# Kernel optimization log

Measured on AMD Instinct MI355X. Metric: run time of the kernel, lower is better.

The kernel has to match this reference:

```python
import jax, jax.numpy as jnp
import numpy as np

B, T, E, H = 32, 256, 1024, 1024


def setup_inputs() -> dict:
    key = jax.random.key(0)
    ks = jax.random.split(key, 8)
    stdv = 1.0 / np.sqrt(H)
    u = lambda k, shape: jax.random.uniform(k, shape, jnp.float32, -stdv, stdv)
    return {
        "x": jax.random.normal(ks[0], (B, T, E), jnp.float32),
        "mask": jnp.ones((B, T), jnp.float32),
        "W_ih0": u(ks[1], (E, 4 * H)),
        "W_hh0": u(ks[2], (H, 4 * H)),
        "b0": jnp.zeros((4 * H,), jnp.float32),
        "W_ih1": u(ks[3], (H, 4 * H)),
        "W_hh1": u(ks[4], (H, 4 * H)),
        "b1": jnp.zeros((4 * H,), jnp.float32),
    }


def _cell(inp, m_t, h0, c0, Wih, Whh, b):
    # pre-activations: [B, 4H]; gate order f, i, o, g (as in torch.split)
    pre = inp @ Wih + h0 @ Whh + b
    f, i, o, g = jnp.split(pre, 4, axis=1)
    m = m_t[:, None]
    c1 = jax.nn.sigmoid(f) * c0 + jax.nn.sigmoid(i) * jnp.tanh(g)
    c1 = c1 * m + c0 * (1.0 - m)
    h1 = jax.nn.sigmoid(o) * jnp.tanh(c1)
    h1 = h1 * m + h0 * (1.0 - m)
    return h1, c1


def reference(x, mask, W_ih0, W_hh0, b0, W_ih1, W_hh1, b1):
    Bz = x.shape[0]
    Hd = W_hh0.shape[0]

    def step(carry, xm):
        h0, c0, h1, c1 = carry
        xt, mt = xm
        # NOTE: layer 1 consumes PREVIOUS timestep's layer-0 hidden (source quirk)
        nh1, nc1 = _cell(h0, mt, h1, c1, W_ih1, W_hh1, b1)
        nh0, nc0 = _cell(xt, mt, h0, c0, W_ih0, W_hh0, b0)
        return (nh0, nc0, nh1, nc1), nh1

    z = jnp.zeros((Bz, Hd), x.dtype)
    init = (z, z, z, z)
    xs = (jnp.swapaxes(x, 0, 1), jnp.swapaxes(mask, 0, 1))  # [T,B,E], [T,B]
    _, hs = jax.lax.scan(step, init, xs)  # hs: [T, B, H]
    states = jnp.swapaxes(hs, 0, 1)  # [B, T, H]
    return states, mask
```

## Files before the change

kernel.cpp:

```cpp
#include <hip/hip_runtime.h>
#include <hip/hip_bf16.h>
#include <stdint.h>
#include <stddef.h>

#define TT    256
#define NBLK  128

typedef __attribute__((ext_vector_type(8))) short short8;
typedef __attribute__((ext_vector_type(4))) float f32x4;

__device__ __forceinline__ short f2bf(float v) {
  uint32_t u = __builtin_bit_cast(uint32_t, v);
  uint32_t r = (u + 0x7fffu + ((u >> 16) & 1u)) >> 16;
  return (short)r;
}

__device__ __forceinline__ void stage_coh(const short8* g, short8* l) {
  __builtin_amdgcn_global_load_lds(
      (const __attribute__((address_space(1))) void*)g,
      (__attribute__((address_space(3))) void*)l, 16, 0, 17);
}
__device__ __forceinline__ void stage_pln(const short8* g, short8* l) {
  __builtin_amdgcn_global_load_lds(
      (const __attribute__((address_space(1))) void*)g,
      (__attribute__((address_space(3))) void*)l, 16, 0, 0);
}

__device__ __forceinline__ void spin_lines(const uint32_t* baseA, uint32_t tgtA,
                                           const uint32_t* baseB, uint32_t tgtB,
                                           int lane) {
  const uint32_t* p = (lane < 32 ? baseA : baseB) + (lane & 15) * 32;
  const uint32_t tgt = (lane < 32) ? tgtA : tgtB;
  for (;;) {
    uint32_t v = __hip_atomic_load(p, __ATOMIC_RELAXED, __HIP_MEMORY_SCOPE_AGENT);
    if (__all(v >= tgt)) break;
    __builtin_amdgcn_s_sleep(1);
  }
}

__global__ void k_init(const float* __restrict__ mask, float* __restrict__ out,
                       uint32_t* __restrict__ z) {
  int tid = blockIdx.x * blockDim.x + threadIdx.x;
  if (tid < 8192) out[8388608 + tid] = mask[tid];
  for (int j = tid; j < 51200; j += 16384) z[j] = 0;
}

__global__ void k_packw(const float* __restrict__ Wih0, const float* __restrict__ Whh0,
                        const float* __restrict__ Wih1, const float* __restrict__ Whh1,
                        short* __restrict__ Bp) {
  int cid = blockIdx.x * blockDim.x + threadIdx.x;
  int l    = cid & 63;
  int f    = (cid >> 6) & 63;
  int wgid = cid >> 12;
  int q  = l >> 4, cc = l & 15;
  int cg = f >> 4, s = f & 15;
  int w    = wgid & 3;
  int blk  = (wgid >> 2) & 63;
  bool p1  = (wgid >= 256);
  int precol = (cc >> 2) * 1024 + blk * 16 + cg * 4 + (cc & 3);
  const float* MA = p1 ? Wih1 : Wih0;
  const float* MB = p1 ? Whh1 : Whh0;
  short8 o;
#pragma unroll
  for (int j = 0; j < 8; ++j) {
    int k = w * 512 + s * 32 + q * 8 + j;
    const float* M = (k < 1024) ? MA : MB;
    o[j] = f2bf(M[(size_t)(k & 1023) * 4096 + precol]);
  }
  ((short8*)Bp)[cid] = o;
}

__global__ void k_packx(const float* __restrict__ x, short* __restrict__ Xb) {
  int tid = blockIdx.x * blockDim.x + threadIdx.x;
  int eg = tid & 127;
  int t  = (tid >> 7) & 255;
  int b  = tid >> 15;
  const float* src = x + ((size_t)(b * 256 + t) * 1024 + eg * 8);
  short8 o;
#pragma unroll
  for (int j = 0; j < 8; ++j) o[j] = f2bf(src[j]);
  ((short8*)Xb)[(t * 128 + eg) * 32 + b] = o;
}

__global__ __launch_bounds__(256, 1) void k_lstm(
    const float* __restrict__ mask, const float* __restrict__ b0,
    const float* __restrict__ b1,   const short* __restrict__ Bp,
    const short* __restrict__ Xb,   short* __restrict__ h0r,
    short* __restrict__ h1b,        float* __restrict__ out,
    uint32_t* bar) {
  __shared__ short8 stg[8192];
  __shared__ f32x4 xch[4][3][2][64];
  __shared__ short hstage[512];

  const int tid  = threadIdx.x;
  const int wv   = tid >> 6;
  const int lane = tid & 63;
  const int quad = lane >> 4;
  const int cc   = lane & 15;
  const int bid  = blockIdx.x;
  const bool is1 = (bid >= 64);
  const int blk  = bid & 63;
  const int wgid = (is1 ? 256 : 0) + blk * 4 + wv;
  const int n0w  = blk * 16 + wv * 4;
  const int hcol = n0w + (cc & 3);
  const int kb0  = (wv & 1) * 64;
  const bool coh = !(!is1 && wv < 2);

  uint32_t* const lines0 = bar;
  uint32_t* const lines1 = bar + 1024;
  uint32_t* const arrC   = (is1 ? lines1 : lines0) + (blk & 15) * 32;

  short8 bfr[64];
  {
    const short8* pB = ((const short8*)Bp) + (size_t)wgid * 4096 + lane;
#pragma unroll
    for (int f = 0; f < 64; ++f) bfr[f] = pB[f * 64];
  }
  const float* bias = is1 ? b1 : b0;
  const float bv = bias[(cc >> 2) * 1024 + n0w + (cc & 3)];

  float cst[8], hst[8];
#pragma unroll
  for (int i = 0; i < 8; ++i) { cst[i] = 0.f; hst[i] = 0.f; }

  const int shuf_base = (lane & 48) | (lane & 3);
  const short8* Xq = (const short8*)Xb;
  const short8* H0 = (const short8*)h0r;
  const short8* H1 = (const short8*)h1b;

  short8* const ldsW = stg + wv * 2048;

  const int tmax = is1 ? TT : (TT - 1);

  for (int t = 0; t < tmax; ++t) {
    const int p  = t & 1;
    const int rs = (t + 127) & 127;

    const short8* pan;
    if (!is1) pan = (wv < 2) ? (Xq + (size_t)t * 4096) : (H0 + (size_t)rs * 4096);
    else      pan = (wv < 2) ? (H0 + (size_t)rs * 4096) : (H1 + p * 4096);

    float mrow[8];
#pragma unroll
    for (int i = 0; i < 8; ++i) {
      int r = ((i >> 2) << 4) + quad * 4 + (i & 3);
      mrow[i] = mask[r * 256 + t];
    }

    if (t > 0) {
      const uint32_t tgt = (uint32_t)(4 * t);
      if (!is1) {
        if (wv >= 2) {
          uint32_t tgtB = (t >= 127) ? (uint32_t)(4 * (t - 126)) : 0u;
          spin_lines(lines0, tgt, lines1, tgtB, lane);
        }
      } else {
        if (wv < 2) spin_lines(lines0, tgt, lines0, tgt, lane);
        else        spin_lines(lines1, tgt, lines1, tgt, lane);
      }
    }

    {
      const short8* gsrc = pan + kb0 * 32 + lane;
      if (coh) {
#pragma unroll
        for (int i = 0; i < 32; ++i) stage_coh(gsrc + i * 64, ldsW + i * 64);
      } else {
#pragma unroll
        for (int i = 0; i < 32; ++i) stage_pln(gsrc + i * 64, ldsW + i * 64);
      }
      asm volatile("s_waitcnt vmcnt(0)" ::: "memory");
      __builtin_amdgcn_sched_barrier(0);
    }

    f32x4 acc[4][2];
#pragma unroll
    for (int cg = 0; cg < 4; ++cg) { acc[cg][0] = (f32x4)0.f; acc[cg][1] = (f32x4)0.f; }

#pragma unroll
    for (int s = 0; s < 16; ++s) {
      short8 a0 = ldsW[(s * 4 + quad) * 32 + cc];
      short8 a1 = ldsW[(s * 4 + quad) * 32 + cc + 16];
#pragma unroll
      for (int cg = 0; cg < 4; ++cg) {
        acc[cg][0] = __builtin_amdgcn_mfma_f32_16x16x32_bf16(a0, bfr[cg * 16 + s], acc[cg][0], 0, 0, 0);
        acc[cg][1] = __builtin_amdgcn_mfma_f32_16x16x32_bf16(a1, bfr[cg * 16 + s], acc[cg][1], 0, 0, 0);
      }
    }

#pragma unroll
    for (int cg = 0; cg < 4; ++cg) {
      if (cg != wv) {
        int slot = cg < wv ? cg : cg - 1;
        xch[wv][slot][0][lane] = acc[cg][0];
        xch[wv][slot][1][lane] = acc[cg][1];
      }
    }
    __syncthreads();
    f32x4 s0 = acc[wv][0], s1 = acc[wv][1];
#pragma unroll
    for (int w2 = 0; w2 < 4; ++w2) {
      if (w2 != wv) {
        int slot = wv < w2 ? wv : wv - 1;
        s0 += xch[w2][slot][0][lane];
        s1 += xch[w2][slot][1][lane];
      }
    }

    float pv[8];
    pv[0] = s0.x + bv; pv[1] = s0.y + bv; pv[2] = s0.z + bv; pv[3] = s0.w + bv;
    pv[4] = s1.x + bv; pv[5] = s1.y + bv; pv[6] = s1.z + bv; pv[7] = s1.w + bv;

#pragma unroll
    for (int i = 0; i < 8; ++i) {
      float v = pv[i];
      float fg = __shfl(v, shuf_base + 0, 64);
      float ig = __shfl(v, shuf_base + 4, 64);
      float og = __shfl(v, shuf_base + 8, 64);
      float gg = __shfl(v, shuf_base + 12, 64);
      int r = ((i >> 2) << 4) + quad * 4 + (i & 3);
      float m  = mrow[i];
      float om = 1.f - m;
      float sf = 1.f / (1.f + __expf(-fg));
      float si = 1.f / (1.f + __expf(-ig));
      float so = 1.f / (1.f + __expf(-og));
      float e2 = __expf(-2.f * fabsf(gg));
      float tg = (1.f - e2) / (1.f + e2);
      tg = (gg < 0.f) ? -tg : tg;
      float c1 = sf * cst[i] + si * tg;
      c1 = c1 * m + cst[i] * om;
      float ec = __expf(-2.f * fabsf(c1));
      float tc = (1.f - ec) / (1.f + ec);
      tc = (c1 < 0.f) ? -tc : tc;
      float h1 = so * tc;
      h1 = h1 * m + hst[i] * om;
      cst[i] = c1; hst[i] = h1;
      if ((lane & 12) == 0) {
        int hl = wv * 4 + (cc & 3);
        hstage[(hl >> 3) * 256 + r * 8 + (hl & 7)] = f2bf(h1);
        if (is1) out[((size_t)r * 256 + t) * 1024 + hcol] = h1;
      }
    }

    if (is1 && t == TT - 1) break;

    __syncthreads();
    if (wv == 0) {
      short* dst = (is1 ? (h1b + (1 - p) * 32768)
                        : (h0r + (t & 127) * 32768)) + blk * 512 + lane * 8;
      short8 hv = ((const short8*)hstage)[lane];
      asm volatile("global_store_dwordx4 %0, %1, off sc0 sc1"
                   :: "v"(dst), "v"(hv) : "memory");
      if (lane == 0) {
        asm volatile("s_waitcnt vmcnt(0)" ::: "memory");
        __hip_atomic_fetch_add(arrC, 1u, __ATOMIC_RELAXED, __HIP_MEMORY_SCOPE_AGENT);
      }
    }
  }
}

extern "C" void kernel_launch(void* const* d_in, const int* in_sizes, int n_in,
                              void* d_out, int out_size, void* d_ws, size_t ws_size,
                              hipStream_t stream) {
  const float* x    = (const float*)d_in[0];
  const float* mask = (const float*)d_in[1];
  const float* Wih0 = (const float*)d_in[2];
  const float* Whh0 = (const float*)d_in[3];
  const float* b0   = (const float*)d_in[4];
  const float* Wih1 = (const float*)d_in[5];
  const float* Whh1 = (const float*)d_in[6];
  const float* b1   = (const float*)d_in[7];
  float* out = (float*)d_out;

  char* ws = (char*)d_ws;
  short*    Bp  = (short*)ws;
  short*    Xb  = (short*)(ws + 33554432);
  short*    h0r = (short*)(ws + 50331648);
  short*    h1b = (short*)(ws + 58720256);
  uint32_t* bar = (uint32_t*)(ws + 58851328);
  uint32_t* z   = (uint32_t*)(ws + 58654720);

  hipLaunchKernelGGL(k_init,  dim3(64),   dim3(256), 0, stream, mask, out, z);
  hipLaunchKernelGGL(k_packw, dim3(8192), dim3(256), 0, stream, Wih0, Whh0, Wih1, Whh1, Bp);
  hipLaunchKernelGGL(k_packx, dim3(4096), dim3(256), 0, stream, x, Xb);
  hipLaunchKernelGGL(k_lstm,  dim3(NBLK), dim3(256), 0, stream,
                     mask, b0, b1, Bp, Xb, h0r, h1b, out, bar);
}
```

Before: 2.555 ms.

## Replace coherent staging loads with ring buffers plus periodic acquire fence

The h1 buffer grows from a 2-entry double buffer into a 32-slot ring. All LDS staging loads now use plain cached global_load_lds instead of the coherent (sc-bit) variant. An agent-scope acquire fence every 32 steps invalidates stale cache lines, since each ring slot is only reused after 32 steps. This trades per-load cache bypass for an occasional fence and more workspace. It relies on the h0 ring (128 slots) and h1 ring (32 slots) never being served stale from cache between fences, which is a fragile memory-model assumption.

Result: faster. 2.475 ms (-3.1%).

```diff
diff --git a/kernel.cpp b/kernel.cpp
--- a/kernel.cpp
+++ b/kernel.cpp
@@ -15,12 +15,7 @@
   return (short)r;
 }
 
-__device__ __forceinline__ void stage_coh(const short8* g, short8* l) {
-  __builtin_amdgcn_global_load_lds(
-      (const __attribute__((address_space(1))) void*)g,
-      (__attribute__((address_space(3))) void*)l, 16, 0, 17);
-}
-__device__ __forceinline__ void stage_pln(const short8* g, short8* l) {
+__device__ __forceinline__ void stage16(const short8* g, short8* l) {
   __builtin_amdgcn_global_load_lds(
       (const __attribute__((address_space(1))) void*)g,
       (__attribute__((address_space(3))) void*)l, 16, 0, 0);
@@ -39,10 +34,12 @@
 }
 
 __global__ void k_init(const float* __restrict__ mask, float* __restrict__ out,
-                       uint32_t* __restrict__ z) {
+                       uint32_t* __restrict__ wsu) {
   int tid = blockIdx.x * blockDim.x + threadIdx.x;
   if (tid < 8192) out[8388608 + tid] = mask[tid];
-  for (int j = tid; j < 51200; j += 16384) z[j] = 0;
+  wsu[14663680 + tid] = 0;
+  wsu[15187968 + tid] = 0;
+  if (tid < 2048) wsu[15204352 + tid] = 0;
 }
 
 __global__ void k_packw(const float* __restrict__ Wih0, const float* __restrict__ Whh0,
@@ -104,7 +101,6 @@
   const int n0w  = blk * 16 + wv * 4;
   const int hcol = n0w + (cc & 3);
   const int kb0  = (wv & 1) * 64;
-  const bool coh = !(!is1 && wv < 2);
 
   uint32_t* const lines0 = bar;
   uint32_t* const lines1 = bar + 1024;
@@ -133,12 +129,13 @@
   const int tmax = is1 ? TT : (TT - 1);
 
   for (int t = 0; t < tmax; ++t) {
-    const int p  = t & 1;
+    const int p  = t & 31;
     const int rs = (t + 127) & 127;
+    const int r1 = (t + 31) & 31;
 
     const short8* pan;
     if (!is1) pan = (wv < 2) ? (Xq + (size_t)t * 4096) : (H0 + (size_t)rs * 4096);
-    else      pan = (wv < 2) ? (H0 + (size_t)rs * 4096) : (H1 + p * 4096);
+    else      pan = (wv < 2) ? (H0 + (size_t)rs * 4096) : (H1 + (size_t)r1 * 4096);
 
     float mrow[8];
 #pragma unroll
@@ -160,15 +157,12 @@
       }
     }
 
+    if ((t & 31) == 1) __builtin_amdgcn_fence(__ATOMIC_ACQUIRE, "agent");
+
     {
       const short8* gsrc = pan + kb0 * 32 + lane;
-      if (coh) {
-#pragma unroll
-        for (int i = 0; i < 32; ++i) stage_coh(gsrc + i * 64, ldsW + i * 64);
-      } else {
-#pragma unroll
-        for (int i = 0; i < 32; ++i) stage_pln(gsrc + i * 64, ldsW + i * 64);
-      }
+#pragma unroll
+      for (int i = 0; i < 32; ++i) stage16(gsrc + i * 64, ldsW + i * 64);
       asm volatile("s_waitcnt vmcnt(0)" ::: "memory");
       __builtin_amdgcn_sched_barrier(0);
     }
@@ -246,8 +240,8 @@
 
     __syncthreads();
     if (wv == 0) {
-      short* dst = (is1 ? (h1b + (1 - p) * 32768)
-                        : (h0r + (t & 127) * 32768)) + blk * 512 + lane * 8;
+      short* dst = (is1 ? (h1b + (size_t)p * 32768)
+                        : (h0r + (size_t)(t & 127) * 32768)) + blk * 512 + lane * 8;
       short8 hv = ((const short8*)hstage)[lane];
       asm volatile("global_store_dwordx4 %0, %1, off sc0 sc1"
                    :: "v"(dst), "v"(hv) : "memory");
@@ -277,10 +271,9 @@
   short*    Xb  = (short*)(ws + 33554432);
   short*    h0r = (short*)(ws + 50331648);
   short*    h1b = (short*)(ws + 58720256);
-  uint32_t* bar = (uint32_t*)(ws + 58851328);
-  uint32_t* z   = (uint32_t*)(ws + 58654720);
-
-  hipLaunchKernelGGL(k_init,  dim3(64),   dim3(256), 0, stream, mask, out, z);
+  uint32_t* bar = (uint32_t*)(ws + 60817408);
+
+  hipLaunchKernelGGL(k_init,  dim3(64),   dim3(256), 0, stream, mask, out, (uint32_t*)ws);
   hipLaunchKernelGGL(k_packw, dim3(8192), dim3(256), 0, stream, Wih0, Whh0, Wih1, Whh1, Bp);
   hipLaunchKernelGGL(k_packx, dim3(4096), dim3(256), 0, stream, x, Xb);
   hipLaunchKernelGGL(k_lstm,  dim3(NBLK), dim3(256), 0, stream,
```
